# Optimization experiments

Hardware: AMD Instinct MI355X
Metric: run time of the kernel (lower is better)

## Reference

```python
import jax, jax.numpy as jnp
import numpy as np

L, D, H, EXP = 6, 512, 8, 4
DH = D // H
EPS = 1e-3  # keras LayerNormalization default epsilon


def _layer_norm(x, gamma, beta):
    mu = jnp.mean(x, axis=-1, keepdims=True)
    var = jnp.mean(jnp.square(x - mu), axis=-1, keepdims=True)
    return (x - mu) * jax.lax.rsqrt(var + EPS) * gamma + beta


def setup_inputs() -> dict:
    key = jax.random.key(0)
    ks = jax.random.split(key, 10)
    B, S = 8, 1024
    s_attn = 1.0 / np.sqrt(D)
    s_ffn1 = 1.0 / np.sqrt(D)
    s_ffn2 = 1.0 / np.sqrt(D * EXP)
    return {
        "x": jax.random.normal(ks[0], (B, S, D), dtype=jnp.float32),
        "Wq": jax.random.normal(ks[1], (L, D, D), dtype=jnp.float32) * s_attn,
        "Wk": jax.random.normal(ks[2], (L, D, D), dtype=jnp.float32) * s_attn,
        "Wv": jax.random.normal(ks[3], (L, D, D), dtype=jnp.float32) * s_attn,
        "Wo": jax.random.normal(ks[4], (L, D, D), dtype=jnp.float32) * s_attn,
        "W1": jax.random.normal(ks[5], (L, D, D * EXP), dtype=jnp.float32) * s_ffn1,
        "b1": jnp.zeros((L, D * EXP), dtype=jnp.float32),
        "W2": jax.random.normal(ks[6], (L, D * EXP, D), dtype=jnp.float32) * s_ffn2,
        "b2": jnp.zeros((L, D), dtype=jnp.float32),
        "g_attn": jnp.ones((L, D), dtype=jnp.float32),
        "be_attn": jnp.zeros((L, D), dtype=jnp.float32),
        "g_ffn": jnp.ones((L, D), dtype=jnp.float32),
        "be_ffn": jnp.zeros((L, D), dtype=jnp.float32),
    }


def _self_attention(y, wq, wk, wv, wo):
    B, S, _ = y.shape
    q = (y @ wq).reshape(B, S, H, DH)
    k = (y @ wk).reshape(B, S, H, DH)
    v = (y @ wv).reshape(B, S, H, DH)
    scores = jnp.einsum("bqhd,bkhd->bhqk", q, k) / np.sqrt(float(DH))
    attn = jax.nn.softmax(scores, axis=-1)
    z = jnp.einsum("bhqk,bkhd->bqhd", attn, v).reshape(B, S, D)
    return z @ wo


def reference(x, Wq, Wk, Wv, Wo, W1, b1, W2, b2, g_attn, be_attn, g_ffn, be_ffn):
    encoded = x
    for l in range(L):
        # pre-LN self-attention + residual (dropout=identity at inference)
        attended = _layer_norm(encoded, g_attn[l], be_attn[l])
        attended = _self_attention(attended, Wq[l], Wk[l], Wv[l], Wo[l])
        attended = encoded + attended
        # pre-LN FFN + residual
        h = _layer_norm(attended, g_ffn[l], be_ffn[l])
        h = jax.nn.relu(h @ W1[l] + b1[l]) @ W2[l] + b2[l]
        encoded = attended + h
    return encoded
```

## Files before the change

kernel.cpp:

```cpp
#include <hip/hip_runtime.h>


#define SEQ 1024
#define ROWS 8192
#define QKVW 1536

using bf16x8 = __attribute__((ext_vector_type(8))) short;
using f32x4  = __attribute__((ext_vector_type(4))) float;

__device__ __forceinline__ unsigned short f2bf(float f) {
  union { float f; unsigned u; } v; v.f = f;
  unsigned r = v.u + 0x7FFFu + ((v.u >> 16) & 1u);
  return (unsigned short)(r >> 16);
}

__device__ __forceinline__ float exp2_fast(float x) {
  float r;
  asm("v_exp_f32 %0, %1" : "=v"(r) : "v"(x));
  return r;
}

__device__ __forceinline__ unsigned cvtpk_bf16(float a, float b) {
  unsigned r;
  asm("v_cvt_pk_bf16_f32 %0, %1, %2" : "=v"(r) : "v"(a), "v"(b));
  return r;
}

__device__ __forceinline__ void gl16(const void* g, void* l) {
  typedef const unsigned int __attribute__((address_space(1)))* GP;
  typedef unsigned int __attribute__((address_space(3)))* LP;
  __builtin_amdgcn_global_load_lds((GP)g, (LP)l, 16, 0, 0);
}

__global__ __launch_bounds__(256) void transpose_cast_k(
    const float* __restrict__ W, unsigned short* __restrict__ Wt,
    int K, int N, int lstride, float scale)
{
  __shared__ float tile[32][33];
  const int l = blockIdx.z;
  const float* Wl = W + (size_t)l * K * N;
  unsigned short* Wtl = Wt + (size_t)l * lstride;
  const int k0 = blockIdx.y * 32, n0 = blockIdx.x * 32;
  const int tx = threadIdx.x & 31, ty = threadIdx.x >> 5;
  #pragma unroll
  for (int i = ty; i < 32; i += 8)
    tile[i][tx] = Wl[(size_t)(k0 + i) * N + n0 + tx];
  __syncthreads();
  #pragma unroll
  for (int i = ty; i < 32; i += 8)
    Wtl[(size_t)(n0 + i) * K + k0 + tx] = f2bf(tile[tx][i] * scale);
}

__global__ __launch_bounds__(256) void ln_k(
    const float* __restrict__ x, const float* __restrict__ g,
    const float* __restrict__ be, unsigned short* __restrict__ y, int rows)
{
  const int wid = (blockIdx.x << 2) | (threadIdx.x >> 6);
  const int lane = threadIdx.x & 63;
  if (wid >= rows) return;
  const float4* xr = reinterpret_cast<const float4*>(x + (size_t)wid * 512);
  float4 a = xr[lane];
  float4 b = xr[lane + 64];
  float s = a.x + a.y + a.z + a.w + b.x + b.y + b.z + b.w;
  #pragma unroll
  for (int m = 32; m >= 1; m >>= 1) s += __shfl_xor(s, m);
  const float mu = s * (1.0f / 512.0f);
  const float d0 = a.x - mu, d1 = a.y - mu, d2 = a.z - mu, d3 = a.w - mu;
  const float e0 = b.x - mu, e1 = b.y - mu, e2 = b.z - mu, e3 = b.w - mu;
  float q = d0*d0 + d1*d1 + d2*d2 + d3*d3 + e0*e0 + e1*e1 + e2*e2 + e3*e3;
  #pragma unroll
  for (int m = 32; m >= 1; m >>= 1) q += __shfl_xor(q, m);
  const float inv = rsqrtf(q * (1.0f / 512.0f) + 1e-3f);
  const float4* gr = reinterpret_cast<const float4*>(g);
  const float4* br = reinterpret_cast<const float4*>(be);
  const float4 g0 = gr[lane], g1 = gr[lane + 64];
  const float4 h0 = br[lane], h1 = br[lane + 64];
  ushort4 o0, o1;
  o0.x = f2bf(d0 * inv * g0.x + h0.x);
  o0.y = f2bf(d1 * inv * g0.y + h0.y);
  o0.z = f2bf(d2 * inv * g0.z + h0.z);
  o0.w = f2bf(d3 * inv * g0.w + h0.w);
  o1.x = f2bf(e0 * inv * g1.x + h1.x);
  o1.y = f2bf(e1 * inv * g1.y + h1.y);
  o1.z = f2bf(e2 * inv * g1.z + h1.z);
  o1.w = f2bf(e3 * inv * g1.w + h1.w);
  *reinterpret_cast<ushort4*>(y + (size_t)wid * 512 + lane * 4) = o0;
  *reinterpret_cast<ushort4*>(y + (size_t)wid * 512 + (lane + 64) * 4) = o1;
}

template<bool RELU, bool HASBIAS, bool HASRES, bool OUTBF>
__global__ __launch_bounds__(256) void gemm128_k(
    const unsigned short* __restrict__ A,
    const unsigned short* __restrict__ Wt,
    const float* __restrict__ bias,
    const float* __restrict__ res,
    void* __restrict__ outp, int M, int N, int K)
{
  __shared__ __align__(16) unsigned short As0[4096], Bs0[4096];
  __shared__ __align__(16) unsigned short As1[4096], Bs1[4096];
  const int t = threadIdx.x;
  const int nwg = gridDim.x * gridDim.y;
  const int bid = blockIdx.y * gridDim.x + blockIdx.x;
  const int nid = (bid & 7) * (nwg >> 3) + (bid >> 3);
  const int bx = nid % gridDim.x, by = nid / gridDim.x;
  const int m0 = by * 128, n0 = bx * 128;
  const int w = t >> 6, lane = t & 63, llo = lane & 15, lhi = lane >> 4;
  const int wr = w >> 1, wc = w & 1;

  const int sr = t >> 2, sg = (t & 3) ^ ((t >> 3) & 3);
  const unsigned short* pa = &A[(size_t)(m0 + sr) * K + sg * 8];
  const unsigned short* pb = &Wt[(size_t)(n0 + sr) * K + sg * 8];

#define GSTAGE128(AsX, BsX, koff) do { \
    gl16(pa + (koff), &AsX[t * 8]); \
    gl16(pa + (size_t)64 * K + (koff), &AsX[2048 + t * 8]); \
    gl16(pb + (koff), &BsX[t * 8]); \
    gl16(pb + (size_t)64 * K + (koff), &BsX[2048 + t * 8]); \
  } while (0)

  const int pgo = (lhi ^ ((llo >> 1) & 3)) * 8;

#define GCOMP128(AsX, BsX) do { \
    bf16x8 af[4], bfr[4]; \
    _Pragma("unroll") \
    for (int f = 0; f < 4; f++) { \
      af[f]  = *reinterpret_cast<const bf16x8*>(&AsX[(wr * 64 + f * 16 + llo) * 32 + pgo]); \
      bfr[f] = *reinterpret_cast<const bf16x8*>(&BsX[(wc * 64 + f * 16 + llo) * 32 + pgo]); \
    } \
    _Pragma("unroll") \
    for (int fi = 0; fi < 4; fi++) \
      _Pragma("unroll") \
      for (int fj = 0; fj < 4; fj++) \
        acc[fi][fj] = __builtin_amdgcn_mfma_f32_16x16x32_bf16(af[fi], bfr[fj], acc[fi][fj], 0, 0, 0); \
  } while (0)

  f32x4 acc[4][4] = {};
  GSTAGE128(As0, Bs0, 0);
  for (int k0 = 0; k0 < K; k0 += 64) {
    __syncthreads();
    GSTAGE128(As1, Bs1, k0 + 32);
    GCOMP128(As0, Bs0);
    __syncthreads();
    if (k0 + 64 < K) GSTAGE128(As0, Bs0, k0 + 64);
    GCOMP128(As1, Bs1);
  }
#undef GSTAGE128
#undef GCOMP128

  const int row0 = m0 + wr * 64, col0 = n0 + wc * 64;
  #pragma unroll
  for (int fi = 0; fi < 4; fi++)
    #pragma unroll
    for (int fj = 0; fj < 4; fj++)
      #pragma unroll
      for (int i = 0; i < 4; i++) {
        const int row = row0 + fi * 16 + lhi * 4 + i;
        const int col = col0 + fj * 16 + llo;
        float v = acc[fi][fj][i];
        if (HASBIAS) v += bias[col];
        if (HASRES)  v += res[(size_t)row * N + col];
        if (RELU)    v = fmaxf(v, 0.0f);
        if (OUTBF) ((unsigned short*)outp)[(size_t)row * N + col] = f2bf(v);
        else       ((float*)outp)[(size_t)row * N + col] = v;
      }
}

template<bool RELU, bool HASBIAS, bool HASRES, bool OUTBF>
__global__ __launch_bounds__(256) void gemm64_k(
    const unsigned short* __restrict__ A,
    const unsigned short* __restrict__ Wt,
    const float* __restrict__ bias,
    const float* __restrict__ res,
    void* __restrict__ outp, int M, int N, int K)
{
  __shared__ __align__(16) unsigned short As0[2048], Bs0[4096];
  __shared__ __align__(16) unsigned short As1[2048], Bs1[4096];
  const int t = threadIdx.x;
  const int nwg = gridDim.x * gridDim.y;
  const int bid = blockIdx.y * gridDim.x + blockIdx.x;
  const int nid = (bid & 7) * (nwg >> 3) + (bid >> 3);
  const int bx = nid % gridDim.x, by = nid / gridDim.x;
  const int m0 = by * 64, n0 = bx * 128;
  const int w = t >> 6, lane = t & 63, llo = lane & 15, lhi = lane >> 4;
  const int wr = w >> 1, wc = w & 1;

  const int sr = t >> 2, sg = (t & 3) ^ ((t >> 3) & 3);
  const unsigned short* pa = &A[(size_t)(m0 + sr) * K + sg * 8];
  const unsigned short* pb = &Wt[(size_t)(n0 + sr) * K + sg * 8];

#define GSTAGE64(AsX, BsX, koff) do { \
    gl16(pa + (koff), &AsX[t * 8]); \
    gl16(pb + (koff), &BsX[t * 8]); \
    gl16(pb + (size_t)64 * K + (koff), &BsX[2048 + t * 8]); \
  } while (0)

  const int pgo = (lhi ^ ((llo >> 1) & 3)) * 8;

#define GCOMP64(AsX, BsX) do { \
    bf16x8 af[2], bfr[4]; \
    _Pragma("unroll") \
    for (int f = 0; f < 2; f++) \
      af[f] = *reinterpret_cast<const bf16x8*>(&AsX[(wr * 32 + f * 16 + llo) * 32 + pgo]); \
    _Pragma("unroll") \
    for (int f = 0; f < 4; f++) \
      bfr[f] = *reinterpret_cast<const bf16x8*>(&BsX[(wc * 64 + f * 16 + llo) * 32 + pgo]); \
    _Pragma("unroll") \
    for (int fi = 0; fi < 2; fi++) \
      _Pragma("unroll") \
      for (int fj = 0; fj < 4; fj++) \
        acc[fi][fj] = __builtin_amdgcn_mfma_f32_16x16x32_bf16(af[fi], bfr[fj], acc[fi][fj], 0, 0, 0); \
  } while (0)

  f32x4 acc[2][4] = {};
  GSTAGE64(As0, Bs0, 0);
  for (int k0 = 0; k0 < K; k0 += 64) {
    __syncthreads();
    GSTAGE64(As1, Bs1, k0 + 32);
    GCOMP64(As0, Bs0);
    __syncthreads();
    if (k0 + 64 < K) GSTAGE64(As0, Bs0, k0 + 64);
    GCOMP64(As1, Bs1);
  }
#undef GSTAGE64
#undef GCOMP64

  const int row0 = m0 + wr * 32, col0 = n0 + wc * 64;
  #pragma unroll
  for (int fi = 0; fi < 2; fi++)
    #pragma unroll
    for (int fj = 0; fj < 4; fj++)
      #pragma unroll
      for (int i = 0; i < 4; i++) {
        const int row = row0 + fi * 16 + lhi * 4 + i;
        const int col = col0 + fj * 16 + llo;
        float v = acc[fi][fj][i];
        if (HASBIAS) v += bias[col];
        if (HASRES)  v += res[(size_t)row * N + col];
        if (RELU)    v = fmaxf(v, 0.0f);
        if (OUTBF) ((unsigned short*)outp)[(size_t)row * N + col] = f2bf(v);
        else       ((float*)outp)[(size_t)row * N + col] = v;
      }
}

__global__ __launch_bounds__(256) void vtrans_k(
    const unsigned short* __restrict__ QKV, unsigned short* __restrict__ VT)
{
  __shared__ unsigned short tile[64][66];
  const int kt = blockIdx.x, bh = blockIdx.y;
  const int bb = bh >> 3, h = bh & 7;
  const int t = threadIdx.x;
  const int r = t >> 2, c0 = (t & 3) * 16;
  const unsigned short* src = &QKV[((size_t)bb * SEQ + kt * 64 + r) * QKVW + 1024 + h * 64 + c0];
  *reinterpret_cast<uint4*>(&tile[r][c0])     = *reinterpret_cast<const uint4*>(src);
  *reinterpret_cast<uint4*>(&tile[r][c0 + 8]) = *reinterpret_cast<const uint4*>(src + 8);
  __syncthreads();
  const int dv = t >> 2, kv0 = (t & 3) * 16;
  unsigned short tmp[16];
  #pragma unroll
  for (int j = 0; j < 16; j++) tmp[j] = tile[kv0 + j][dv];
  ushort4 o0, o1, o2, o3;
  o0.x = tmp[0];  o0.y = tmp[1];  o0.z = tmp[2];  o0.w = tmp[3];
  o1.x = tmp[4];  o1.y = tmp[5];  o1.z = tmp[6];  o1.w = tmp[7];
  o2.x = tmp[8];  o2.y = tmp[9];  o2.z = tmp[10]; o2.w = tmp[11];
  o3.x = tmp[12]; o3.y = tmp[13]; o3.z = tmp[14]; o3.w = tmp[15];
  unsigned short* dst = &VT[((size_t)bh * 64 + dv) * SEQ + kt * 64 + kv0];
  *reinterpret_cast<ushort4*>(dst)      = o0;
  *reinterpret_cast<ushort4*>(dst + 4)  = o1;
  *reinterpret_cast<ushort4*>(dst + 8)  = o2;
  *reinterpret_cast<ushort4*>(dst + 12) = o3;
}

__global__ __launch_bounds__(256) void attn_k(
    const unsigned short* __restrict__ QKV,
    const unsigned short* __restrict__ VT,
    unsigned short* __restrict__ Zb)
{
  __shared__ __align__(16) unsigned short Ks0[4096], Vs0[4096];
  __shared__ __align__(16) unsigned short Ks1[4096], Vs1[4096];
  __shared__ __align__(16) unsigned short Ps[8192];

  const int t = threadIdx.x;
  const int h = blockIdx.x, qt = blockIdx.y, bb = blockIdx.z;
  const int w = t >> 6, lane = t & 63, llo = lane & 15, lhi = lane >> 4;
  const size_t rowb = (size_t)bb * SEQ;
  const int kcol = 512 + h * 64;
  const size_t vtb = (size_t)(bb * 8 + h) * 64 * SEQ;

  bf16x8 aq[2][2];
  #pragma unroll
  for (int mi = 0; mi < 2; mi++)
    #pragma unroll
    for (int ds = 0; ds < 2; ds++)
      aq[mi][ds] = *reinterpret_cast<const bf16x8*>(
          &QKV[(rowb + qt * 128 + w * 32 + mi * 16 + llo) * QKVW + h * 64 + ds * 32 + lhi * 8]);

  const int cA = t, cB = 256 + t;
  const int gA = cA >> 6, lA = cA & 63, gB = cB >> 6, lB = cB & 63;
  const unsigned short* kpA = &QKV[(rowb + (gA >> 1) * 16 + (lA & 15)) * QKVW + kcol + (gA & 1) * 32 + (lA >> 4) * 8];
  const unsigned short* kpB = &QKV[(rowb + (gB >> 1) * 16 + (lB & 15)) * QKVW + kcol + (gB & 1) * 32 + (lB >> 4) * 8];
  const unsigned short* vpA = &VT[vtb + (size_t)((gA >> 1) * 16 + (lA & 15)) * SEQ + (gA & 1) * 32 + (lA >> 4) * 8];
  const unsigned short* vpB = &VT[vtb + (size_t)((gB >> 1) * 16 + (lB & 15)) * SEQ + (gB & 1) * 32 + (lB >> 4) * 8];

#define ASTAGE(KsX, VsX, ktt) do { \
    gl16(kpA + (size_t)(ktt) * 64 * QKVW, &KsX[cA * 8]); \
    gl16(kpB + (size_t)(ktt) * 64 * QKVW, &KsX[cB * 8]); \
    gl16(vpA + (ktt) * 64, &VsX[cA * 8]); \
    gl16(vpB + (ktt) * 64, &VsX[cB * 8]); \
  } while (0)

  const int psw = w * 2048;
  const int lsw = llo & 7;

#define ACOMP(KsX, VsX) do { \
    f32x4 s_[2][4]; \
    _Pragma("unroll") \
    for (int mi = 0; mi < 2; mi++) \
      _Pragma("unroll") \
      for (int fj = 0; fj < 4; fj++) \
        _Pragma("unroll") \
        for (int i = 0; i < 4; i++) s_[mi][fj][i] = -16.0f; \
    _Pragma("unroll") \
    for (int ds = 0; ds < 2; ds++) \
      _Pragma("unroll") \
      for (int fj = 0; fj < 4; fj++) { \
        bf16x8 bk = *reinterpret_cast<const bf16x8*>(&KsX[((fj * 2 + ds) * 64 + lane) * 8]); \
        s_[0][fj] = __builtin_amdgcn_mfma_f32_16x16x32_bf16(bk, aq[0][ds], s_[0][fj], 0, 0, 0); \
        s_[1][fj] = __builtin_amdgcn_mfma_f32_16x16x32_bf16(bk, aq[1][ds], s_[1][fj], 0, 0, 0); \
      } \
    _Pragma("unroll") \
    for (int mi = 0; mi < 2; mi++) \
      _Pragma("unroll") \
      for (int fj = 0; fj < 4; fj++) { \
        const float p0 = exp2_fast(s_[mi][fj][0]); \
        const float p1 = exp2_fast(s_[mi][fj][1]); \
        const float p2 = exp2_fast(s_[mi][fj][2]); \
        const float p3 = exp2_fast(s_[mi][fj][3]); \
        l_[mi] += (p0 + p1) + (p2 + p3); \
        uint2 uv; uv.x = cvtpk_bf16(p0, p1); uv.y = cvtpk_bf16(p2, p3); \
        const int pg = ((fj << 1) | (lhi >> 1)) ^ lsw; \
        *reinterpret_cast<uint2*>(&Ps[psw + (mi * 16 + llo) * 64 + pg * 8 + (lhi & 1) * 4]) = uv; \
      } \
    _Pragma("unroll") \
    for (int ks = 0; ks < 2; ks++) { \
      const int prg = (((ks << 2) | lhi) ^ lsw) << 3; \
      bf16x8 ap0 = *reinterpret_cast<const bf16x8*>(&Ps[psw + llo * 64 + prg]); \
      bf16x8 ap1 = *reinterpret_cast<const bf16x8*>(&Ps[psw + (16 + llo) * 64 + prg]); \
      _Pragma("unroll") \
      for (int fo = 0; fo < 4; fo++) { \
        bf16x8 bv = *reinterpret_cast<const bf16x8*>(&VsX[((fo * 2 + ks) * 64 + lane) * 8]); \
        o_[0][fo] = __builtin_amdgcn_mfma_f32_16x16x32_bf16(ap0, bv, o_[0][fo], 0, 0, 0); \
        o_[1][fo] = __builtin_amdgcn_mfma_f32_16x16x32_bf16(ap1, bv, o_[1][fo], 0, 0, 0); \
      } \
    } \
  } while (0)

  float l_[2] = {0.0f, 0.0f};
  f32x4 o_[2][4] = {};

  ASTAGE(Ks0, Vs0, 0);
  for (int kt = 0; kt < 16; kt += 2) {
    __syncthreads();
    ASTAGE(Ks1, Vs1, kt + 1);
    ACOMP(Ks0, Vs0);
    __syncthreads();
    if (kt + 2 < 16) ASTAGE(Ks0, Vs0, kt + 2);
    ACOMP(Ks1, Vs1);
  }
#undef ASTAGE
#undef ACOMP

  #pragma unroll
  for (int mi = 0; mi < 2; mi++) {
    l_[mi] += __shfl_xor(l_[mi], 16);
    l_[mi] += __shfl_xor(l_[mi], 32);
    l_[mi] = 1.0f / l_[mi];
  }

  #pragma unroll
  for (int mi = 0; mi < 2; mi++)
    #pragma unroll
    for (int i = 0; i < 4; i++) {
      const float li = __shfl(l_[mi], lhi * 4 + i);
      #pragma unroll
      for (int fo = 0; fo < 4; fo++) {
        const float v = o_[mi][fo][i] * li;
        Zb[(rowb + qt * 128 + w * 32 + mi * 16 + lhi * 4 + i) * 512 + h * 64 + fo * 16 + llo] = f2bf(v);
      }
    }
}

extern "C" void kernel_launch(void* const* d_in, const int* in_sizes, int n_in,
                              void* d_out, int out_size, void* d_ws, size_t ws_size,
                              hipStream_t stream)
{
  const float* x   = (const float*)d_in[0];
  const float* Wq  = (const float*)d_in[1];
  const float* Wk  = (const float*)d_in[2];
  const float* Wv  = (const float*)d_in[3];
  const float* Wo  = (const float*)d_in[4];
  const float* W1  = (const float*)d_in[5];
  const float* b1  = (const float*)d_in[6];
  const float* W2  = (const float*)d_in[7];
  const float* b2  = (const float*)d_in[8];
  const float* ga  = (const float*)d_in[9];
  const float* ba  = (const float*)d_in[10];
  const float* gf  = (const float*)d_in[11];
  const float* bfn = (const float*)d_in[12];
  float* out = (float*)d_out;

  char* p = (char*)d_ws;
  auto alloc = [&](size_t bytes) { void* r = (void*)p; p += (bytes + 255) & ~(size_t)255; return r; };
  float* E0 = (float*)alloc((size_t)ROWS * 512 * 4);
  float* E1 = (float*)alloc((size_t)ROWS * 512 * 4);
  unsigned short* Ybf   = (unsigned short*)alloc((size_t)ROWS * 512 * 2);
  unsigned short* QKVbf = (unsigned short*)alloc((size_t)ROWS * QKVW * 2);
  unsigned short* H1bf  = (unsigned short*)alloc((size_t)ROWS * 2048 * 2);
  unsigned short* VT    = H1bf;
  unsigned short* WtQKV = (unsigned short*)alloc(6ull * QKVW * 512 * 2);
  unsigned short* WtO   = (unsigned short*)alloc(6ull * 512 * 512 * 2);
  unsigned short* Wt1   = (unsigned short*)alloc(6ull * 2048 * 512 * 2);
  unsigned short* Wt2   = (unsigned short*)alloc(6ull * 512 * 2048 * 2);
  unsigned short* Zbf   = Ybf;

  const float qscale = 0.125f * 1.44269504f;
  transpose_cast_k<<<dim3(16, 16, 6), 256, 0, stream>>>(Wq, WtQKV,          512, 512,  QKVW * 512, qscale);
  transpose_cast_k<<<dim3(16, 16, 6), 256, 0, stream>>>(Wk, WtQKV + 262144, 512, 512,  QKVW * 512, 1.0f);
  transpose_cast_k<<<dim3(16, 16, 6), 256, 0, stream>>>(Wv, WtQKV + 524288, 512, 512,  QKVW * 512, 1.0f);
  transpose_cast_k<<<dim3(16, 16, 6), 256, 0, stream>>>(Wo, WtO,            512, 512,  262144,     1.0f);
  transpose_cast_k<<<dim3(64, 16, 6), 256, 0, stream>>>(W1, Wt1,            512, 2048, 1048576,    1.0f);
  transpose_cast_k<<<dim3(16, 64, 6), 256, 0, stream>>>(W2, Wt2,            2048, 512, 1048576,    1.0f);

  for (int l = 0; l < 6; l++) {
    const float* enc = (l == 0) ? x : E0;
    ln_k<<<2048, 256, 0, stream>>>(enc, ga + l * 512, ba + l * 512, Ybf, ROWS);
    gemm128_k<false, false, false, true><<<dim3(12, 64), 256, 0, stream>>>(
        Ybf, WtQKV + (size_t)l * QKVW * 512, nullptr, nullptr, QKVbf, ROWS, QKVW, 512);
    vtrans_k<<<dim3(16, 64), 256, 0, stream>>>(QKVbf, VT);
    attn_k<<<dim3(8, 8, 8), 256, 0, stream>>>(QKVbf, VT, Zbf);
    gemm64_k<false, false, true, false><<<dim3(4, 128), 256, 0, stream>>>(
        Zbf, WtO + (size_t)l * 262144, nullptr, enc, E1, ROWS, 512, 512);
    ln_k<<<2048, 256, 0, stream>>>(E1, gf + l * 512, bfn + l * 512, Ybf, ROWS);
    gemm128_k<true, true, false, true><<<dim3(16, 64), 256, 0, stream>>>(
        Ybf, Wt1 + (size_t)l * 1048576, b1 + l * 2048, nullptr, H1bf, ROWS, 2048, 512);
    gemm64_k<false, true, true, false><<<dim3(4, 128), 256, 0, stream>>>(
        H1bf, Wt2 + (size_t)l * 1048576, b2 + l * 512, E1, (l == 5) ? out : E0,
        ROWS, 512, 2048);
  }
}
```

Before: 818.4 us.

## Split-K the FFN down-projection and fold partial sums into next layer norm

The FFN second GEMM (K=2048, only 512 workgroups) is split into two K halves over blockIdx.z, doubling the grid to raise occupancy on the many CUs. Each half writes an fp32 partial (bias added to one). The next layer's attention LayerNorm kernel is replaced by a fused kernel that sums the residual and both partials, writes the encoded tensor and normalizes. This costs extra fp32 traffic for two partial buffers (P1 aliases the QKV buffer) in exchange for better parallelism. The last layer keeps the original path.

```diff
diff --git a/kernel.cpp b/kernel.cpp
--- a/kernel.cpp
+++ b/kernel.cpp
@@ -88,6 +88,52 @@
   *reinterpret_cast<ushort4*>(y + (size_t)wid * 512 + (lane + 64) * 4) = o1;
 }
 
+__global__ __launch_bounds__(256) void ln_sum_k(
+    const float* __restrict__ x1, const float* __restrict__ p0,
+    const float* __restrict__ p1, const float* __restrict__ g,
+    const float* __restrict__ be, unsigned short* __restrict__ y,
+    float* __restrict__ e0, int rows)
+{
+  const int wid = (blockIdx.x << 2) | (threadIdx.x >> 6);
+  const int lane = threadIdx.x & 63;
+  if (wid >= rows) return;
+  const float4* xr = reinterpret_cast<const float4*>(x1 + (size_t)wid * 512);
+  const float4* pr0 = reinterpret_cast<const float4*>(p0 + (size_t)wid * 512);
+  const float4* pr1 = reinterpret_cast<const float4*>(p1 + (size_t)wid * 512);
+  float4 a = xr[lane], b = xr[lane + 64];
+  const float4 u0 = pr0[lane], u1 = pr0[lane + 64];
+  const float4 v0 = pr1[lane], v1 = pr1[lane + 64];
+  a.x += u0.x + v0.x; a.y += u0.y + v0.y; a.z += u0.z + v0.z; a.w += u0.w + v0.w;
+  b.x += u1.x + v1.x; b.y += u1.y + v1.y; b.z += u1.z + v1.z; b.w += u1.w + v1.w;
+  float4* er = reinterpret_cast<float4*>(e0 + (size_t)wid * 512);
+  er[lane] = a; er[lane + 64] = b;
+  float s = a.x + a.y + a.z + a.w + b.x + b.y + b.z + b.w;
+  #pragma unroll
+  for (int m = 32; m >= 1; m >>= 1) s += __shfl_xor(s, m);
+  const float mu = s * (1.0f / 512.0f);
+  const float d0 = a.x - mu, d1 = a.y - mu, d2 = a.z - mu, d3 = a.w - mu;
+  const float e0_ = b.x - mu, e1_ = b.y - mu, e2_ = b.z - mu, e3_ = b.w - mu;
+  float q = d0*d0 + d1*d1 + d2*d2 + d3*d3 + e0_*e0_ + e1_*e1_ + e2_*e2_ + e3_*e3_;
+  #pragma unroll
+  for (int m = 32; m >= 1; m >>= 1) q += __shfl_xor(q, m);
+  const float inv = rsqrtf(q * (1.0f / 512.0f) + 1e-3f);
+  const float4* gr = reinterpret_cast<const float4*>(g);
+  const float4* br = reinterpret_cast<const float4*>(be);
+  const float4 g0 = gr[lane], g1 = gr[lane + 64];
+  const float4 h0 = br[lane], h1 = br[lane + 64];
+  ushort4 o0, o1;
+  o0.x = f2bf(d0 * inv * g0.x + h0.x);
+  o0.y = f2bf(d1 * inv * g0.y + h0.y);
+  o0.z = f2bf(d2 * inv * g0.z + h0.z);
+  o0.w = f2bf(d3 * inv * g0.w + h0.w);
+  o1.x = f2bf(e0_ * inv * g1.x + h1.x);
+  o1.y = f2bf(e1_ * inv * g1.y + h1.y);
+  o1.z = f2bf(e2_ * inv * g1.z + h1.z);
+  o1.w = f2bf(e3_ * inv * g1.w + h1.w);
+  *reinterpret_cast<ushort4*>(y + (size_t)wid * 512 + lane * 4) = o0;
+  *reinterpret_cast<ushort4*>(y + (size_t)wid * 512 + (lane + 64) * 4) = o1;
+}
+
 template<bool RELU, bool HASBIAS, bool HASRES, bool OUTBF>
 __global__ __launch_bounds__(256) void gemm128_k(
     const unsigned short* __restrict__ A,
@@ -242,6 +288,83 @@
       }
 }
 
+__global__ __launch_bounds__(256) void gemm64s_k(
+    const unsigned short* __restrict__ A,
+    const unsigned short* __restrict__ Wt,
+    const float* __restrict__ bias,
+    float* __restrict__ o0, float* __restrict__ o1,
+    int M, int N, int Kstride, int Kloop)
+{
+  __shared__ __align__(16) unsigned short As0[2048], Bs0[4096];
+  __shared__ __align__(16) unsigned short As1[2048], Bs1[4096];
+  const int t = threadIdx.x;
+  const int z = blockIdx.z;
+  A  += (size_t)z * Kloop;
+  Wt += (size_t)z * Kloop;
+  const int nwg = gridDim.x * gridDim.y;
+  const int bid = blockIdx.y * gridDim.x + blockIdx.x;
+  const int nid = (bid & 7) * (nwg >> 3) + (bid >> 3);
+  const int bx = nid % gridDim.x, by = nid / gridDim.x;
+  const int m0 = by * 64, n0 = bx * 128;
+  const int w = t >> 6, lane = t & 63, llo = lane & 15, lhi = lane >> 4;
+  const int wr = w >> 1, wc = w & 1;
+
+  const int sr = t >> 2, sg = (t & 3) ^ ((t >> 3) & 3);
+  const unsigned short* pa = &A[(size_t)(m0 + sr) * Kstride + sg * 8];
+  const unsigned short* pb = &Wt[(size_t)(n0 + sr) * Kstride + sg * 8];
+
+#define GSTAGE64S(AsX, BsX, koff) do { \
+    gl16(pa + (koff), &AsX[t * 8]); \
+    gl16(pb + (koff), &BsX[t * 8]); \
+    gl16(pb + (size_t)64 * Kstride + (koff), &BsX[2048 + t * 8]); \
+  } while (0)
+
+  const int pgo = (lhi ^ ((llo >> 1) & 3)) * 8;
+
+#define GCOMP64S(AsX, BsX) do { \
+    bf16x8 af[2], bfr[4]; \
+    _Pragma("unroll") \
+    for (int f = 0; f < 2; f++) \
+      af[f] = *reinterpret_cast<const bf16x8*>(&AsX[(wr * 32 + f * 16 + llo) * 32 + pgo]); \
+    _Pragma("unroll") \
+    for (int f = 0; f < 4; f++) \
+      bfr[f] = *reinterpret_cast<const bf16x8*>(&BsX[(wc * 64 + f * 16 + llo) * 32 + pgo]); \
+    _Pragma("unroll") \
+    for (int fi = 0; fi < 2; fi++) \
+      _Pragma("unroll") \
+      for (int fj = 0; fj < 4; fj++) \
+        acc[fi][fj] = __builtin_amdgcn_mfma_f32_16x16x32_bf16(af[fi], bfr[fj], acc[fi][fj], 0, 0, 0); \
+  } while (0)
+
+  f32x4 acc[2][4] = {};
+  GSTAGE64S(As0, Bs0, 0);
+  for (int k0 = 0; k0 < Kloop; k0 += 64) {
+    __syncthreads();
+    GSTAGE64S(As1, Bs1, k0 + 32);
+    GCOMP64S(As0, Bs0);
+    __syncthreads();
+    if (k0 + 64 < Kloop) GSTAGE64S(As0, Bs0, k0 + 64);
+    GCOMP64S(As1, Bs1);
+  }
+#undef GSTAGE64S
+#undef GCOMP64S
+
+  float* op = z ? o1 : o0;
+  const int row0 = m0 + wr * 32, col0 = n0 + wc * 64;
+  #pragma unroll
+  for (int fi = 0; fi < 2; fi++)
+    #pragma unroll
+    for (int fj = 0; fj < 4; fj++)
+      #pragma unroll
+      for (int i = 0; i < 4; i++) {
+        const int row = row0 + fi * 16 + lhi * 4 + i;
+        const int col = col0 + fj * 16 + llo;
+        float v = acc[fi][fj][i];
+        if (z == 0) v += bias[col];
+        op[(size_t)row * N + col] = v;
+      }
+}
+
 __global__ __launch_bounds__(256) void vtrans_k(
     const unsigned short* __restrict__ QKV, unsigned short* __restrict__ VT)
 {
@@ -421,6 +544,8 @@
   unsigned short* Wt1   = (unsigned short*)alloc(6ull * 2048 * 512 * 2);
   unsigned short* Wt2   = (unsigned short*)alloc(6ull * 512 * 2048 * 2);
   unsigned short* Zbf   = Ybf;
+  float* P0 = E0;
+  float* P1 = (float*)QKVbf;
 
   const float qscale = 0.125f * 1.44269504f;
   transpose_cast_k<<<dim3(16, 16, 6), 256, 0, stream>>>(Wq, WtQKV,          512, 512,  QKVW * 512, qscale);
@@ -431,8 +556,12 @@
   transpose_cast_k<<<dim3(16, 64, 6), 256, 0, stream>>>(W2, Wt2,            2048, 512, 1048576,    1.0f);
 
   for (int l = 0; l < 6; l++) {
+    if (l == 0)
+      ln_k<<<2048, 256, 0, stream>>>(x, ga, ba, Ybf, ROWS);
+    else
+      ln_sum_k<<<2048, 256, 0, stream>>>(E1, P0, P1, ga + l * 512, ba + l * 512,
+                                         Ybf, E0, ROWS);
     const float* enc = (l == 0) ? x : E0;
-    ln_k<<<2048, 256, 0, stream>>>(enc, ga + l * 512, ba + l * 512, Ybf, ROWS);
     gemm128_k<false, false, false, true><<<dim3(12, 64), 256, 0, stream>>>(
         Ybf, WtQKV + (size_t)l * QKVW * 512, nullptr, nullptr, QKVbf, ROWS, QKVW, 512);
     vtrans_k<<<dim3(16, 64), 256, 0, stream>>>(QKVbf, VT);
@@ -442,8 +571,14 @@
     ln_k<<<2048, 256, 0, stream>>>(E1, gf + l * 512, bfn + l * 512, Ybf, ROWS);
     gemm128_k<true, true, false, true><<<dim3(16, 64), 256, 0, stream>>>(
         Ybf, Wt1 + (size_t)l * 1048576, b1 + l * 2048, nullptr, H1bf, ROWS, 2048, 512);
-    gemm64_k<false, true, true, false><<<dim3(4, 128), 256, 0, stream>>>(
-        H1bf, Wt2 + (size_t)l * 1048576, b2 + l * 512, E1, (l == 5) ? out : E0,
-        ROWS, 512, 2048);
+    if (l < 5) {
+      gemm64s_k<<<dim3(4, 128, 2), 256, 0, stream>>>(
+          H1bf, Wt2 + (size_t)l * 1048576, b2 + l * 512, P0, P1,
+          ROWS, 512, 2048, 1024);
+    } else {
+      gemm64_k<false, true, true, false><<<dim3(4, 128), 256, 0, stream>>>(
+          H1bf, Wt2 + (size_t)l * 1048576, b2 + l * 512, E1, out,
+          ROWS, 512, 2048);
+    }
   }
 }
```

After: 873.0 us. 1.07x slower.
